# Kernel optimization log

Measured on AMD Instinct MI355X. Metric: run time of the kernel, lower is better.

## Reference

```python
import jax, jax.numpy as jnp
import numpy as np

EPS = 1e-5  # torch BatchNorm1d default eps


def setup_inputs() -> dict:
    key = jax.random.key(0)
    ks = jax.random.split(key, 8)
    F, P = 32, 64            # frames, peds per frame
    B = F * P                # batch = 2048
    E, H, M, D = 64, 128, 512, 1024  # embed, h_dim, pool_mlp_dim, bottleneck
    starts = np.arange(F, dtype=np.int64) * P
    seq_start_end = jnp.asarray(np.stack([starts, starts + P], axis=1))
    inp = {
        "curr_h_states": jax.random.normal(ks[0], (1, B, H), dtype=jnp.float32),
        "curr_pos": jax.random.normal(ks[1], (B, 2), dtype=jnp.float32),
        "seq_start_end": seq_start_end,
        # embedding: Linear(2, E)
        "We": jax.random.normal(ks[2], (2, E), dtype=jnp.float32) * 0.5,
        "be": jnp.zeros((E,), dtype=jnp.float32),
        # mlp layer 1: Linear(E+H, M) + BN(M)
        "W1": jax.random.normal(ks[3], (E + H, M), dtype=jnp.float32) * 0.05,
        "b1": jnp.zeros((M,), dtype=jnp.float32),
        "g1": jnp.ones((M,), dtype=jnp.float32),
        "beta1": jnp.zeros((M,), dtype=jnp.float32),
        # mlp layer 2: Linear(M, D) + BN(D)
        "W2": jax.random.normal(ks[4], (M, D), dtype=jnp.float32) * 0.04,
        "b2": jnp.zeros((D,), dtype=jnp.float32),
        "g2": jnp.ones((D,), dtype=jnp.float32),
        "beta2": jnp.zeros((D,), dtype=jnp.float32),
        # BN running stats (eval mode)
        "rm1": jnp.zeros((M,), dtype=jnp.float32),
        "rv1": jnp.ones((M,), dtype=jnp.float32),
        "rm2": jnp.zeros((D,), dtype=jnp.float32),
        "rv2": jnp.ones((D,), dtype=jnp.float32),
    }
    return inp


def _bn(x, g, beta, rm, rv):
    return g * (x - rm) * jax.lax.rsqrt(rv + EPS) + beta


def reference(curr_h_states, curr_pos, seq_start_end, We, be, W1, b1, g1, beta1,
              W2, b2, g2, beta2, rm1, rv1, rm2, rv2):
    # Equal-size frames: vectorize the per-frame Python loop via a reshape.
    F = seq_start_end.shape[0]
    B = curr_h_states.shape[1]
    P = B // F
    h = curr_h_states[0].reshape(F, P, -1)      # (F, P, H)
    pos = curr_pos.reshape(F, P, 2)             # (F, P, 2)
    # rel_pos[f, i, j] = pos[f, j] - pos[f, i]  (repeat minus repeat_interleave)
    rel = pos[:, None, :, :] - pos[:, :, None, :]          # (F, P, P, 2)
    emb = rel @ We + be                                     # (F, P, P, E)
    h_rep = jnp.broadcast_to(h[:, None, :, :], (F, P, P, h.shape[-1]))
    x = jnp.concatenate([emb, h_rep], axis=-1)              # (F, P, P, E+H)
    x = jax.nn.relu(_bn(x @ W1 + b1, g1, beta1, rm1, rv1))  # (F, P, P, M)
    x = jax.nn.relu(_bn(x @ W2 + b2, g2, beta2, rm2, rv2))  # (F, P, P, D)
    pool_h = x.max(axis=2)                                  # max over j -> (F, P, D)
    return pool_h.reshape(B, -1)                            # (B, D)
```

## Files before the change

### kernel.cpp

```cpp
#include <hip/hip_runtime.h>
#include <hip/hip_bf16.h>
#include <stdint.h>

#define EPS_BN 1e-5f

constexpr int Fn = 32;
constexpr int Pn = 64;
constexpr int Bn = 2048;
constexpr int Hn = 128;
constexpr int En = 64;
constexpr int Mn = 512;
constexpr int Dn = 1024;

using bf16x8  = __attribute__((ext_vector_type(8))) short;
using f32x16  = __attribute__((ext_vector_type(16))) float;

static __device__ __forceinline__ float    bcf(uint32_t u) { return __builtin_bit_cast(float, u); }
static __device__ __forceinline__ uint32_t bcu(float f)    { return __builtin_bit_cast(uint32_t, f); }
static __device__ __forceinline__ unsigned short bfbits(float f) {
  return __builtin_bit_cast(unsigned short, __float2bfloat16(f));
}

static __device__ __forceinline__ void dma16(const uint4* g, const uint4* l) {
  __builtin_amdgcn_global_load_lds(
      (const __attribute__((address_space(1))) unsigned int*)g,
      (__attribute__((address_space(3))) unsigned int*)l, 16, 0, 0);
}

static __device__ __forceinline__ void mk2(uint4 a0, uint4 a1, uint4 q,
                                           bf16x8& r0, bf16x8& r1) {
  uint4 x0, x1;
#pragma unroll
  for (int v = 0; v < 4; ++v) {
    uint32_t qw  = ((const uint32_t*)&q)[v];
    uint32_t a0w = ((const uint32_t*)&a0)[v], a1w = ((const uint32_t*)&a1)[v];
    float qlo = bcf(qw << 16);
    float m0lo = fmaxf(bcf(a0w << 16), qlo);
    float m1lo = fmaxf(bcf(a1w << 16), qlo);
    float m0hi = fmaxf(bcf(a0w), bcf(qw));
    float m1hi = fmaxf(bcf(a1w), bcf(qw));
    ((uint32_t*)&x0)[v] = __builtin_amdgcn_perm(bcu(m0hi), bcu(m0lo), 0x07060302u);
    ((uint32_t*)&x1)[v] = __builtin_amdgcn_perm(bcu(m1hi), bcu(m1lo), 0x07060302u);
  }
  r0 = __builtin_bit_cast(bf16x8, x0);
  r1 = __builtin_bit_cast(bf16x8, x1);
}

__global__ void prep_all(const float* __restrict__ hs, const float* __restrict__ pos,
                         const float* __restrict__ We, const float* __restrict__ be,
                         const float* __restrict__ W1, const float* __restrict__ b1,
                         const float* __restrict__ g1, const float* __restrict__ beta1,
                         const float* __restrict__ rm1, const float* __restrict__ rv1,
                         const float* __restrict__ W2, const float* __restrict__ b2,
                         const float* __restrict__ g2, const float* __restrict__ beta2,
                         const float* __restrict__ rm2, const float* __restrict__ rv2,
                         __hip_bfloat16* __restrict__ Agb, __hip_bfloat16* __restrict__ Qgb,
                         uint4* __restrict__ W2g, float* __restrict__ G0,
                         float* __restrict__ G1, float* __restrict__ c2) {
  __shared__ float smem[64 * 65];
  int bid = blockIdx.x, t = threadIdx.x;
  if (bid < 128) {
    int rb = bid * 16, m = t;
    float* hsh = smem;
    float* psh = smem + 2048;
#pragma unroll
    for (int r4 = 0; r4 < 4; ++r4) hsh[r4 * 512 + t] = hs[rb * Hn + r4 * 512 + t];
    if (t < 32) psh[t] = pos[rb * 2 + t];
    __syncthreads();
    float w0 = 0.f, w1 = 0.f, c = 0.f;
    for (int e = 0; e < En; ++e) {
      float w = W1[e * Mn + m];
      w0 += We[e] * w; w1 += We[En + e] * w; c += be[e] * w;
    }
    c += b1[m];
    float s  = g1[m] * rsqrtf(rv1[m] + EPS_BN);
    float tt = beta1[m] - rm1[m] * s;
    float acc[16];
#pragma unroll
    for (int ri = 0; ri < 16; ++ri) acc[ri] = c;
    for (int e = 0; e < Hn; ++e) {
      float w = W1[(En + e) * Mn + m];
#pragma unroll
      for (int ri = 0; ri < 16; ++ri) acc[ri] += hsh[ri * Hn + e] * w;
    }
#pragma unroll
    for (int ri = 0; ri < 16; ++ri) {
      float q = psh[ri * 2] * w0 + psh[ri * 2 + 1] * w1;
      Agb[(rb + ri) * Mn + m] = __float2bfloat16((acc[ri] + q) * s + tt);
      Qgb[(rb + ri) * Mn + m] = __float2bfloat16(q * s);
    }
  } else if (bid < 256) {
    int b2i = bid - 128;
    int d0 = (b2i & 15) * 64, k0 = (b2i >> 4) * 64;
    int col = t & 63, row8 = t >> 6;
#pragma unroll
    for (int rr = 0; rr < 8; ++rr) {
      int row = rr * 8 + row8;
      smem[row * 65 + col] = W2[(k0 + row) * Dn + d0 + col];
    }
    __syncthreads();
    int lane = t & 63, q8 = t >> 6;
    int sel_n = q8 & 1, sel_ks = q8 >> 1;
    int dl = sel_n * 32 + (lane & 31), d = d0 + dl;
    float sf = g2[d] * rsqrtf(rv2[d] + EPS_BN);
    int kb = sel_ks * 16 + (lane >> 5) * 8;
    uint32_t wd[4];
#pragma unroll
    for (int h = 0; h < 4; ++h) {
      uint32_t u0 = bfbits(smem[(kb + 2 * h) * 65 + dl] * sf);
      uint32_t u1 = bfbits(smem[(kb + 2 * h + 1) * 65 + dl] * sf);
      wd[h] = u0 | (u1 << 16);
    }
    int n32 = (d0 >> 5) + sel_n;
    int ks  = (k0 >> 4) + sel_ks;
    W2g[(n32 * 32 + ks) * 64 + lane] = (uint4){wd[0], wd[1], wd[2], wd[3]};
  } else {
    int gb = bid - 256;
    int d0g = gb * 64;
    float* wr0 = smem;
    float* wr1 = smem + 512;
    {
      int m = t;
      float w0 = 0.f, w1 = 0.f;
      for (int e = 0; e < En; ++e) {
        float w = W1[e * Mn + m];
        w0 += We[e] * w; w1 += We[En + e] * w;
      }
      float s = g1[m] * rsqrtf(rv1[m] + EPS_BN);
      wr0[m] = w0 * s; wr1[m] = w1 * s;
    }
    __syncthreads();
    int dl = t & 63, part = t >> 6;
    float p0 = 0.f, p1 = 0.f;
#pragma unroll 4
    for (int mm = 0; mm < 64; ++mm) {
      int m = part * 64 + mm;
      float wv = W2[m * Dn + d0g + dl];
      p0 += wr0[m] * wv; p1 += wr1[m] * wv;
    }
    float* pr = smem + 1024;
    pr[part * 64 + dl] = p0;
    pr[512 + part * 64 + dl] = p1;
    __syncthreads();
    if (t < 128) {
      int which = t >> 6, dd = d0g + (t & 63);
      float s2v = g2[dd] * rsqrtf(rv2[dd] + EPS_BN);
      float sum = 0.f;
#pragma unroll
      for (int pp = 0; pp < 8; ++pp) sum += pr[which * 512 + pp * 64 + (t & 63)];
      (which ? G1 : G0)[dd] = sum * s2v;
      if (which == 0) c2[dd] = b2[dd] * s2v + beta2[dd] - rm2[dd] * s2v;
    }
  }
}

__launch_bounds__(256, 1)
__global__ void gemm_pool(const __hip_bfloat16* __restrict__ Agb,
                          const __hip_bfloat16* __restrict__ Qgb,
                          const uint4* __restrict__ W2g,
                          const float* __restrict__ pos,
                          const float* __restrict__ G0, const float* __restrict__ G1,
                          const float* __restrict__ c2, float* __restrict__ out) {
  __shared__ uint4 SH[3584];

  int rt = blockIdx.x;
  int ct = blockIdx.y;
  int f = rt >> 3, i0 = (rt & 7) * 8;

  int t = threadIdx.x, lane = t & 63, w = t >> 6;

  const uint4* aGL = (const uint4*)(Agb + (size_t)f * Pn * Mn) +
                     (size_t)(lane & 31) * 64 + (lane >> 5);
  const uint4* bGL = W2g + (size_t)(4 * ct) * 32 * 64 + lane;

  auto stageAB = [&](int p) {
    int buf = p & 1;
#pragma unroll
    for (int s2 = 0; s2 < 2; ++s2) {
      int s = w * 2 + s2;
      int ksl = s >> 1, jf = s & 1;
      dma16(aGL + (size_t)jf * 2048 + (p * 4 + ksl) * 2, SH + buf * 512 + s * 64);
    }
#pragma unroll
    for (int s4 = 0; s4 < 4; ++s4) {
      int sb = w * 4 + s4;
      int ksl = sb >> 2, nf = sb & 3;
      dma16(bGL + (nf * 32 + p * 4 + ksl) * 64, SH + 1024 + buf * 1024 + sb * 64);
    }
  };

  dma16((const uint4*)(Qgb + (size_t)(f * Pn + i0 + 2 * w) * Mn) + lane,
        SH + 3072 + (2 * w) * 64);
  dma16((const uint4*)(Qgb + (size_t)(f * Pn + i0 + 2 * w + 1) * Mn) + lane,
        SH + 3072 + (2 * w + 1) * 64);
  stageAB(0);

  f32x16 acc[2][2][4];
#pragma unroll
  for (int ii = 0; ii < 2; ++ii)
#pragma unroll
    for (int jf = 0; jf < 2; ++jf)
#pragma unroll
      for (int nf = 0; nf < 4; ++nf)
        acc[ii][jf][nf] = (f32x16){0.f,0.f,0.f,0.f,0.f,0.f,0.f,0.f,
                                   0.f,0.f,0.f,0.f,0.f,0.f,0.f,0.f};

  int qbA = 3072 + (2 * w) * 64 + (lane >> 5);
  int qbB = qbA + 64;

#pragma unroll 1
  for (int p = 0; p < 8; ++p) {
    __syncthreads();
    if (p < 7) stageAB(p + 1);
    int ab = (p & 1) * 512 + lane;
    int bb = 1024 + (p & 1) * 1024 + lane;

#pragma unroll 2
    for (int ksl = 0; ksl < 4; ++ksl) {
      int ks = p * 4 + ksl;
      uint4 a0 = SH[ab + (ksl * 2 + 0) * 64];
      uint4 a1 = SH[ab + (ksl * 2 + 1) * 64];
      uint4 qA = SH[qbA + ks * 2];
      uint4 qB = SH[qbB + ks * 2];
      bf16x8 afA0, afA1, afB0, afB1;
      mk2(a0, a1, qA, afA0, afA1);
      mk2(a0, a1, qB, afB0, afB1);
#pragma unroll
      for (int nf = 0; nf < 4; ++nf) {
        bf16x8 bg = __builtin_bit_cast(bf16x8, SH[bb + (ksl * 4 + nf) * 64]);
        acc[0][0][nf] = __builtin_amdgcn_mfma_f32_32x32x16_bf16(afA0, bg, acc[0][0][nf], 0, 0, 0);
        acc[0][1][nf] = __builtin_amdgcn_mfma_f32_32x32x16_bf16(afA1, bg, acc[0][1][nf], 0, 0, 0);
        acc[1][0][nf] = __builtin_amdgcn_mfma_f32_32x32x16_bf16(afB0, bg, acc[1][0][nf], 0, 0, 0);
        acc[1][1][nf] = __builtin_amdgcn_mfma_f32_32x32x16_bf16(afB1, bg, acc[1][1][nf], 0, 0, 0);
      }
    }
  }

#pragma unroll
  for (int ii = 0; ii < 2; ++ii) {
    int i = i0 + 2 * w + ii;
    float px = pos[(f * Pn + i) * 2], py = pos[(f * Pn + i) * 2 + 1];
#pragma unroll
    for (int nf = 0; nf < 4; ++nf) {
      float mx = -3.0e38f;
#pragma unroll
      for (int jf = 0; jf < 2; ++jf)
#pragma unroll
        for (int rg = 0; rg < 16; ++rg)
          mx = fmaxf(mx, acc[ii][jf][nf][rg]);
      mx = fmaxf(mx, __shfl_xor(mx, 32));
      if (lane < 32) {
        int d = ct * 128 + nf * 32 + (lane & 31);
        float r = px * G0[d] + py * G1[d];
        out[(f * Pn + i) * Dn + d] = fmaxf(mx - r + c2[d], 0.f);
      }
    }
  }
}

extern "C" void kernel_launch(void* const* d_in, const int* in_sizes, int n_in,
                              void* d_out, int out_size, void* d_ws, size_t ws_size,
                              hipStream_t stream) {
  const float* hs    = (const float*)d_in[0];
  const float* pos   = (const float*)d_in[1];
  const float* We    = (const float*)d_in[3];
  const float* be    = (const float*)d_in[4];
  const float* W1    = (const float*)d_in[5];
  const float* b1    = (const float*)d_in[6];
  const float* g1    = (const float*)d_in[7];
  const float* beta1 = (const float*)d_in[8];
  const float* W2    = (const float*)d_in[9];
  const float* b2    = (const float*)d_in[10];
  const float* g2    = (const float*)d_in[11];
  const float* beta2 = (const float*)d_in[12];
  const float* rm1   = (const float*)d_in[13];
  const float* rv1   = (const float*)d_in[14];
  const float* rm2   = (const float*)d_in[15];
  const float* rv2   = (const float*)d_in[16];

  char* ws = (char*)d_ws;
  float* c2 = (float*)(ws + 0);
  float* G0 = (float*)(ws + 4096);
  float* G1 = (float*)(ws + 8192);
  __hip_bfloat16* Agb = (__hip_bfloat16*)(ws + 12288);
  __hip_bfloat16* Qgb = (__hip_bfloat16*)(ws + 12288 + 2097152);
  uint4* W2g = (uint4*)(ws + 12288 + 2 * 2097152);
  float* out = (float*)d_out;

  prep_all<<<272, 512, 0, stream>>>(hs, pos, We, be, W1, b1, g1, beta1, rm1, rv1,
                                    W2, b2, g2, beta2, rm2, rv2, Agb, Qgb, W2g,
                                    G0, G1, c2);
  gemm_pool<<<dim3(256, 8), 256, 0, stream>>>(Agb, Qgb, W2g, pos, G0, G1, c2, out);
}
```

Baseline: 264.7 us.

## Halve rows per wave in gemm_pool to double occupancy, reorder grid

Each wave now handles one query row instead of two, so the accumulator count per wave halves (8 instead of 16 32x32 tiles). Launch bounds move to 2 blocks per CU, the grid doubles to 4096 blocks, and blockIdx.x now walks column tiles so that blocks for the same frame run next to each other and can share cached A data. The cost is twice as much total staging of A and W2 tiles per output row, which means more global-to-LDS traffic.

Result: faster. 246.4 us (-6.9%).

```diff
diff --git a/kernel.cpp b/kernel.cpp
--- a/kernel.cpp
+++ b/kernel.cpp
@@ -154,20 +154,21 @@
   }
 }
 
-__launch_bounds__(256, 1)
+__launch_bounds__(256, 2)
 __global__ void gemm_pool(const __hip_bfloat16* __restrict__ Agb,
                           const __hip_bfloat16* __restrict__ Qgb,
                           const uint4* __restrict__ W2g,
                           const float* __restrict__ pos,
                           const float* __restrict__ G0, const float* __restrict__ G1,
                           const float* __restrict__ c2, float* __restrict__ out) {
-  __shared__ uint4 SH[3584];
-
-  int rt = blockIdx.x;
-  int ct = blockIdx.y;
-  int f = rt >> 3, i0 = (rt & 7) * 8;
+  __shared__ uint4 SH[3328];
+
+  int ct = blockIdx.x;
+  int rt = blockIdx.y;
+  int f = rt >> 4, i0 = (rt & 15) * 4;
 
   int t = threadIdx.x, lane = t & 63, w = t >> 6;
+  int i = i0 + w;
 
   const uint4* aGL = (const uint4*)(Agb + (size_t)f * Pn * Mn) +
                      (size_t)(lane & 31) * 64 + (lane >> 5);
@@ -175,38 +176,26 @@
 
   auto stageAB = [&](int p) {
     int buf = p & 1;
-#pragma unroll
-    for (int s2 = 0; s2 < 2; ++s2) {
-      int s = w * 2 + s2;
-      int ksl = s >> 1, jf = s & 1;
-      dma16(aGL + (size_t)jf * 2048 + (p * 4 + ksl) * 2, SH + buf * 512 + s * 64);
-    }
-#pragma unroll
-    for (int s4 = 0; s4 < 4; ++s4) {
-      int sb = w * 4 + s4;
-      int ksl = sb >> 2, nf = sb & 3;
-      dma16(bGL + (nf * 32 + p * 4 + ksl) * 64, SH + 1024 + buf * 1024 + sb * 64);
-    }
+    dma16(aGL + (size_t)0 * 2048 + (p * 4 + w) * 2, SH + buf * 512 + (w * 2 + 0) * 64);
+    dma16(aGL + (size_t)1 * 2048 + (p * 4 + w) * 2, SH + buf * 512 + (w * 2 + 1) * 64);
+#pragma unroll
+    for (int nf = 0; nf < 4; ++nf)
+      dma16(bGL + (nf * 32 + p * 4 + w) * 64,
+            SH + 1024 + buf * 1024 + (w * 4 + nf) * 64);
   };
 
-  dma16((const uint4*)(Qgb + (size_t)(f * Pn + i0 + 2 * w) * Mn) + lane,
-        SH + 3072 + (2 * w) * 64);
-  dma16((const uint4*)(Qgb + (size_t)(f * Pn + i0 + 2 * w + 1) * Mn) + lane,
-        SH + 3072 + (2 * w + 1) * 64);
+  dma16((const uint4*)(Qgb + (size_t)(f * Pn + i) * Mn) + lane, SH + 3072 + w * 64);
   stageAB(0);
 
-  f32x16 acc[2][2][4];
-#pragma unroll
-  for (int ii = 0; ii < 2; ++ii)
-#pragma unroll
-    for (int jf = 0; jf < 2; ++jf)
-#pragma unroll
-      for (int nf = 0; nf < 4; ++nf)
-        acc[ii][jf][nf] = (f32x16){0.f,0.f,0.f,0.f,0.f,0.f,0.f,0.f,
-                                   0.f,0.f,0.f,0.f,0.f,0.f,0.f,0.f};
-
-  int qbA = 3072 + (2 * w) * 64 + (lane >> 5);
-  int qbB = qbA + 64;
+  f32x16 acc[2][4];
+#pragma unroll
+  for (int jf = 0; jf < 2; ++jf)
+#pragma unroll
+    for (int nf = 0; nf < 4; ++nf)
+      acc[jf][nf] = (f32x16){0.f,0.f,0.f,0.f,0.f,0.f,0.f,0.f,
+                             0.f,0.f,0.f,0.f,0.f,0.f,0.f,0.f};
+
+  int qb = 3072 + w * 64 + (lane >> 5);
 
 #pragma unroll 1
   for (int p = 0; p < 8; ++p) {
@@ -215,45 +204,37 @@
     int ab = (p & 1) * 512 + lane;
     int bb = 1024 + (p & 1) * 1024 + lane;
 
-#pragma unroll 2
+#pragma unroll
     for (int ksl = 0; ksl < 4; ++ksl) {
       int ks = p * 4 + ksl;
       uint4 a0 = SH[ab + (ksl * 2 + 0) * 64];
       uint4 a1 = SH[ab + (ksl * 2 + 1) * 64];
-      uint4 qA = SH[qbA + ks * 2];
-      uint4 qB = SH[qbB + ks * 2];
-      bf16x8 afA0, afA1, afB0, afB1;
-      mk2(a0, a1, qA, afA0, afA1);
-      mk2(a0, a1, qB, afB0, afB1);
+      uint4 q  = SH[qb + ks * 2];
+      bf16x8 af0, af1;
+      mk2(a0, a1, q, af0, af1);
 #pragma unroll
       for (int nf = 0; nf < 4; ++nf) {
         bf16x8 bg = __builtin_bit_cast(bf16x8, SH[bb + (ksl * 4 + nf) * 64]);
-        acc[0][0][nf] = __builtin_amdgcn_mfma_f32_32x32x16_bf16(afA0, bg, acc[0][0][nf], 0, 0, 0);
-        acc[0][1][nf] = __builtin_amdgcn_mfma_f32_32x32x16_bf16(afA1, bg, acc[0][1][nf], 0, 0, 0);
-        acc[1][0][nf] = __builtin_amdgcn_mfma_f32_32x32x16_bf16(afB0, bg, acc[1][0][nf], 0, 0, 0);
-        acc[1][1][nf] = __builtin_amdgcn_mfma_f32_32x32x16_bf16(afB1, bg, acc[1][1][nf], 0, 0, 0);
+        acc[0][nf] = __builtin_amdgcn_mfma_f32_32x32x16_bf16(af0, bg, acc[0][nf], 0, 0, 0);
+        acc[1][nf] = __builtin_amdgcn_mfma_f32_32x32x16_bf16(af1, bg, acc[1][nf], 0, 0, 0);
       }
     }
   }
 
-#pragma unroll
-  for (int ii = 0; ii < 2; ++ii) {
-    int i = i0 + 2 * w + ii;
-    float px = pos[(f * Pn + i) * 2], py = pos[(f * Pn + i) * 2 + 1];
-#pragma unroll
-    for (int nf = 0; nf < 4; ++nf) {
-      float mx = -3.0e38f;
-#pragma unroll
-      for (int jf = 0; jf < 2; ++jf)
-#pragma unroll
-        for (int rg = 0; rg < 16; ++rg)
-          mx = fmaxf(mx, acc[ii][jf][nf][rg]);
-      mx = fmaxf(mx, __shfl_xor(mx, 32));
-      if (lane < 32) {
-        int d = ct * 128 + nf * 32 + (lane & 31);
-        float r = px * G0[d] + py * G1[d];
-        out[(f * Pn + i) * Dn + d] = fmaxf(mx - r + c2[d], 0.f);
-      }
+  float px = pos[(f * Pn + i) * 2], py = pos[(f * Pn + i) * 2 + 1];
+#pragma unroll
+  for (int nf = 0; nf < 4; ++nf) {
+    float mx = -3.0e38f;
+#pragma unroll
+    for (int jf = 0; jf < 2; ++jf)
+#pragma unroll
+      for (int rg = 0; rg < 16; ++rg)
+        mx = fmaxf(mx, acc[jf][nf][rg]);
+    mx = fmaxf(mx, __shfl_xor(mx, 32));
+    if (lane < 32) {
+      int d = ct * 128 + nf * 32 + (lane & 31);
+      float r = px * G0[d] + py * G1[d];
+      out[(f * Pn + i) * Dn + d] = fmaxf(mx - r + c2[d], 0.f);
     }
   }
 }
@@ -290,5 +271,5 @@
   prep_all<<<272, 512, 0, stream>>>(hs, pos, We, be, W1, b1, g1, beta1, rm1, rv1,
                                     W2, b2, g2, beta2, rm2, rv2, Agb, Qgb, W2g,
                                     G0, G1, c2);
-  gemm_pool<<<dim3(256, 8), 256, 0, stream>>>(Agb, Qgb, W2g, pos, G0, G1, c2, out);
-}
+  gemm_pool<<<dim3(8, 512), 256, 0, stream>>>(Agb, Qgb, W2g, pos, G0, G1, c2, out);
+}
```
